# Kernel optimization log

Measured on AMD Instinct MI355X. Metric: run time of the kernel, lower is better.

The kernel has to match this reference:

```python
import jax, jax.numpy as jnp
import numpy as np

R = 16  # z_dim
_TRIU = np.triu_indices(R, 1)  # static index pair for plucker coords


def plucker_coords(u, v):
    # L2-normalised Plucker coordinates of span{u, v}; last dim r -> r*(r-1)//2
    outer = u[..., :, None] * v[..., None, :]
    anti = outer - jnp.swapaxes(outer, -1, -2)
    pc = anti[..., _TRIU[0], _TRIU[1]]
    nrm = jnp.linalg.norm(pc, axis=-1, keepdims=True)
    return pc / jnp.maximum(nrm, 1e-8)


def setup_inputs() -> dict:
    key = jax.random.key(0)
    ks = jax.random.split(key, 9)
    B, L, D, Z, P, H = 4, 256, 128, 16, 120, 256
    in_dim = 2 * D + 2 * Z + 3 * P + 2  # 650
    h = jax.random.normal(ks[0], (B, L, D), dtype=jnp.float32)
    z = jax.random.normal(ks[1], (B, L, Z), dtype=jnp.float32)
    p = jax.random.normal(ks[2], (B, L, P), dtype=jnp.float32)
    seq_mask = jax.random.randint(ks[3], (B, L), 0, 2).astype(bool)
    canon_mask = jax.random.randint(ks[4], (B, L, L), 0, 2).astype(bool)
    W1 = jax.random.normal(ks[5], (in_dim, H), dtype=jnp.float32) / np.sqrt(in_dim)
    b1 = jnp.zeros((H,), dtype=jnp.float32)
    W2 = jax.random.normal(ks[6], (H, 1), dtype=jnp.float32) / np.sqrt(H)
    b2 = jnp.zeros((1,), dtype=jnp.float32)
    return {"h": h, "z": z, "p": p, "seq_mask": seq_mask, "canon_mask": canon_mask,
            "W1": W1, "b1": b1, "W2": W2, "b2": b2}


def reference(h, z, p, seq_mask, canon_mask, W1, b1, W2, b2):
    B, L, _ = h.shape
    pos = jnp.arange(L, dtype=h.dtype)
    dist = jnp.abs(pos[:, None] - pos[None, :]) / max(L, 1)  # [L, L]
    dist = jnp.broadcast_to(dist[None, :, :, None], (B, L, L, 1))
    canon_f = canon_mask.astype(h.dtype)[..., None]  # [B, L, L, 1]

    h_i = jnp.broadcast_to(h[:, :, None, :], (B, L, L, h.shape[-1]))
    h_j = jnp.broadcast_to(h[:, None, :, :], (B, L, L, h.shape[-1]))
    z_i = jnp.broadcast_to(z[:, :, None, :], (B, L, L, z.shape[-1]))
    z_j = jnp.broadcast_to(z[:, None, :, :], (B, L, L, z.shape[-1]))
    p_i = jnp.broadcast_to(p[:, :, None, :], (B, L, L, p.shape[-1]))
    p_j = jnp.broadcast_to(p[:, None, :, :], (B, L, L, p.shape[-1]))
    p_ij = plucker_coords(z_i, z_j)  # [B, L, L, 120]

    feat = jnp.concatenate([h_i, h_j, z_i, z_j, p_i, p_j, p_ij, dist, canon_f], axis=-1)
    hdn = jax.nn.gelu(feat @ W1 + b1, approximate=False)
    e_pair = (hdn @ W2 + b2)[..., 0]  # [B, L, L]
    e_pair = (e_pair + jnp.swapaxes(e_pair, 1, 2)) * 0.5
    valid = seq_mask[:, :, None] & seq_mask[:, None, :]
    return jnp.where(valid, e_pair, jnp.asarray(30000.0, e_pair.dtype))
```

## Files before the change

### kernel.cpp

```cpp
#include <hip/hip_runtime.h>
#include <hip/hip_bf16.h>
#include <stdint.h>

#define BB     4
#define L_SEQ  256
#define DIM_H  128
#define DIM_Z  16
#define DIM_P  120
#define HID    256
#define TI     16
#define TJ     8
#define NPAIR  (TI*TJ)

typedef __attribute__((ext_vector_type(8))) short short8;
typedef __attribute__((ext_vector_type(4))) float f32x4;

__device__ __forceinline__ int imin(int a, int b){ return a < b ? a : b; }

struct Triu { int a[128]; int b[128]; };
static constexpr Triu make_triu(){
  Triu t{}; int k=0;
  for (int a=0;a<16;a++) for (int b=a+1;b<16;b++){ t.a[k]=a; t.b[k]=b; ++k; }
  for (;k<128;k++){ t.a[k]=0; t.b[k]=0; }
  return t;
}
static constexpr Triu TRIU = make_triu();

__device__ __forceinline__ short f2bf(float f){
  union { __hip_bfloat16 h; short s; } u;
  u.h = __float2bfloat16(f);
  return u.s;
}

__device__ __forceinline__ float bf2f(short s){
  union { float f; uint32_t u; } x;
  x.u = ((uint32_t)(uint16_t)s) << 16;
  return x.f;
}

__device__ __forceinline__ float gelu_fast(float x){
  float s = fmaf(0.42550f, x, 0.5f);
  s = fminf(fmaxf(s, 0.0f), 1.0f);
  return x * s;
}

template<int CTRL>
__device__ __forceinline__ float ror_add(float x){
  int xi = __float_as_int(x);
  int yi = __builtin_amdgcn_update_dpp(xi, xi, CTRL, 0xF, 0xF, false);
  return x + __int_as_float(yi);
}
__device__ __forceinline__ float reduce16(float x){
  x = ror_add<0x121>(x);
  x = ror_add<0x122>(x);
  x = ror_add<0x124>(x);
  x = ror_add<0x128>(x);
  return x;
}

__global__ __launch_bounds__(256) void k_prep(
    const uint32_t* __restrict__ seq_words, const float* __restrict__ W1,
    int* __restrict__ flag, int* __restrict__ vi, int* __restrict__ nv,
    short* __restrict__ W1pT)
{
  const int blk = blockIdx.x, tid = threadIdx.x;
  if (blk < BB){
    const int lane = tid & 63, w = tid >> 6;
    __shared__ int det[4];
    __shared__ int wc[4];
    uint32_t vdet = seq_words[tid] & 0xFFFFFF00u;
    unsigned long long bm = __ballot(vdet != 0u);
    if (lane == 0) det[w] = (bm != 0ull) ? 1 : 0;
    __syncthreads();
    const bool bytes = (det[0] | det[1] | det[2] | det[3]) != 0;
    if (blk == 0 && tid == 0) *flag = bytes ? 1 : 0;

    const int b = blk, i = tid;
    bool s;
    if (bytes) s = ((const unsigned char*)seq_words)[b*L_SEQ + i] != 0;
    else       s = ((const int*)          seq_words)[b*L_SEQ + i] != 0;
    unsigned long long m = __ballot(s);
    if (lane == 0) wc[w] = __popcll(m);
    __syncthreads();
    int base = 0;
    for (int x = 0; x < w; x++) base += wc[x];
    unsigned long long lower = (1ull << lane) - 1ull;
    int pos = base + __popcll(m & lower);
    if (s) vi[b*L_SEQ + pos] = i;
    if (i == 0) nv[b] = wc[0] + wc[1] + wc[2] + wc[3];
  } else {
    int idx = (blk - BB)*256 + tid;
    int k = idx & 127, n = idx >> 7;
    float v = 0.f;
    if (k < 120)      v = W1[(528+k)*HID + n];
    else if (k==120)  v = W1[648*HID + n];
    else if (k==121)  v = W1[649*HID + n];
    W1pT[n*128 + k] = f2bf(v);
  }
}

__global__ __launch_bounds__(256) void k1_precompute(
    const float* __restrict__ hbuf, const float* __restrict__ zbuf, const float* __restrict__ pbuf,
    const float* __restrict__ W1, const float* __restrict__ b1,
    const int* __restrict__ vi, const int* __restrict__ nv,
    float* __restrict__ Ai, float* __restrict__ Cj)
{
  const int bid = (blockIdx.x * 165) & 511;
  const int b = bid >> 7;
  const int p = bid & 127;
  const int nvb = nv[b];
  if (2*p >= nvb) return;
  const int r0 = vi[b*L_SEQ + 2*p];
  const int r1 = vi[b*L_SEQ + imin(2*p + 1, nvb - 1)];
  const size_t g0 = (size_t)(b*L_SEQ + r0), g1 = (size_t)(b*L_SEQ + r1);

  const int hcol = threadIdx.x;
  float a0, a1, c0, c1;
  a0 = a1 = b1[hcol];
  c0 = c1 = 0.f;

  const float* h0 = hbuf + g0*DIM_H;  const float* h1 = hbuf + g1*DIM_H;
  for (int k=0;k<DIM_H;k++){
    float wa = W1[k*HID + hcol], wc = W1[(128+k)*HID + hcol];
    a0 = fmaf(h0[k], wa, a0); c0 = fmaf(h0[k], wc, c0);
    a1 = fmaf(h1[k], wa, a1); c1 = fmaf(h1[k], wc, c1);
  }
  const float* z0 = zbuf + g0*DIM_Z;  const float* z1 = zbuf + g1*DIM_Z;
  for (int k=0;k<DIM_Z;k++){
    float wa = W1[(256+k)*HID + hcol], wc = W1[(272+k)*HID + hcol];
    a0 = fmaf(z0[k], wa, a0); c0 = fmaf(z0[k], wc, c0);
    a1 = fmaf(z1[k], wa, a1); c1 = fmaf(z1[k], wc, c1);
  }
  const float* p0 = pbuf + g0*DIM_P;  const float* p1 = pbuf + g1*DIM_P;
  for (int k=0;k<DIM_P;k++){
    float wa = W1[(288+k)*HID + hcol], wc = W1[(408+k)*HID + hcol];
    a0 = fmaf(p0[k], wa, a0); c0 = fmaf(p0[k], wc, c0);
    a1 = fmaf(p1[k], wa, a1); c1 = fmaf(p1[k], wc, c1);
  }
  Ai[g0*HID + hcol] = a0;  Cj[g0*HID + hcol] = c0;
  Ai[g1*HID + hcol] = a1;  Cj[g1*HID + hcol] = c1;
}

#define PCCOORD(T) f2bf((u[TRIU.a[(T)]]*v[TRIU.b[(T)]] - u[TRIU.b[(T)]]*v[TRIU.a[(T)]])*inv)
#define PC_CHUNK4(BASE) { \
  _Pragma("unroll") \
  for (int c_=0;c_<4;c_++){ \
    _Pragma("unroll") \
    for (int e_=0;e_<8;e_++){ pk[c_][e_] = PCCOORD((BASE) + c_*8 + e_); } } }

__global__ __launch_bounds__(512, 4) void k2_pair(
    const float* __restrict__ zbuf, const void* __restrict__ canon_raw,
    const float* __restrict__ Ai, const float* __restrict__ Cj,
    const short* __restrict__ W1pT, const float* __restrict__ W2,
    const int* __restrict__ flag_p, const int* __restrict__ vi, const int* __restrict__ nv,
    float* __restrict__ e_out)
{
  const int bid = (blockIdx.x * 997) & 2047;
  const int b  = bid >> 9;
  const int it = (bid >> 5) & 15;
  const int jt = bid & 31;
  const int i0 = it*TI, j0 = jt*TJ;
  const int nvb = nv[b];
  if (i0 >= nvb || j0 >= nvb) return;
  const int tid = threadIdx.x, lane = tid & 63, w = tid >> 6;
  const int brow = b*L_SEQ;

  short8 bfrag[2][4];
  {
    int g = lane >> 4, col = lane & 15;
    int n0 = (2*w+0)*16 + col, n1 = (2*w+1)*16 + col;
    #pragma unroll
    for (int ks=0; ks<4; ks++){
      bfrag[0][ks] = *reinterpret_cast<const short8*>(W1pT + n0*128 + ks*32 + g*8);
      bfrag[1][ks] = *reinterpret_cast<const short8*>(W1pT + n1*128 + ks*32 + g*8);
    }
  }

  __shared__ __align__(16) short pc_lds[NPAIR*128];
  __shared__ short ai_lds[TI*264];
  __shared__ short cj_lds[TJ*264];
  __shared__ float z_lds[(TI+TJ)*17];
  __shared__ float w2_lds[HID];
  __shared__ float epart[NPAIR*9];
  __shared__ int io_lds[TI];
  __shared__ int jo_lds[TJ];

  if (tid < TI)              io_lds[tid]    = vi[brow + imin(i0 + tid,      nvb-1)];
  else if (tid < TI+TJ)      jo_lds[tid-TI] = vi[brow + imin(j0 + (tid-TI), nvb-1)];
  __syncthreads();

  for (int idx = tid; idx < TI*HID; idx += 512){ int r = idx>>8, c = idx&255; ai_lds[r*264+c] = f2bf(Ai[(size_t)(brow+io_lds[r])*HID + c]); }
  for (int idx = tid; idx < TJ*HID; idx += 512){ int r = idx>>8, c = idx&255; cj_lds[r*264+c] = f2bf(Cj[(size_t)(brow+jo_lds[r])*HID + c]); }
  for (int idx = tid; idx < TI*DIM_Z; idx += 512){ int r = idx>>4, c = idx&15; z_lds[r*17+c] = zbuf[(size_t)(brow+io_lds[r])*DIM_Z + c]; }
  for (int idx = tid; idx < TJ*DIM_Z; idx += 512){ int r = idx>>4, c = idx&15; z_lds[(TI+r)*17+c] = zbuf[(size_t)(brow+jo_lds[r])*DIM_Z + c]; }
  if (tid < HID) w2_lds[tid] = W2[tid];
  __syncthreads();

  {
    const int p  = tid & 127;
    const int h  = tid >> 7;
    const int il = p >> 3, jl = p & 7;
    float u[16], v[16];
    #pragma unroll
    for (int a=0;a<16;a++) u[a] = z_lds[il*17+a];
    #pragma unroll
    for (int a=0;a<16;a++) v[a] = z_lds[(TI+jl)*17+a];
    float du=0.f, dv=0.f, uv=0.f;
    #pragma unroll
    for (int a=0;a<16;a++){ du=fmaf(u[a],u[a],du); dv=fmaf(v[a],v[a],dv); uv=fmaf(u[a],v[a],uv); }
    float q = fmaxf(du*dv - uv*uv, 1e-16f);
    float inv = __builtin_amdgcn_rsqf(q);

    short8 pk[4];
    if (h == 0)      PC_CHUNK4(0)
    else if (h == 1) PC_CHUNK4(32)
    else if (h == 2) PC_CHUNK4(64)
    else {
      #pragma unroll
      for (int c_=0;c_<3;c_++){
        #pragma unroll
        for (int e_=0;e_<8;e_++){ pk[c_][e_] = PCCOORD(96 + c_*8 + e_); }
      }
      int gi = io_lds[il], gj = jo_lds[jl];
      float dist = fabsf((float)(gi - gj)) * (1.0f/256.0f);
      float canon;
      if (*flag_p) canon = (((const unsigned char*)canon_raw)[(brow+gi)*L_SEQ + gj] != 0) ? 1.f : 0.f;
      else         canon = (((const int*)          canon_raw)[(brow+gi)*L_SEQ + gj] != 0) ? 1.f : 0.f;
      short8 last;
      last[0] = f2bf(dist); last[1] = f2bf(canon);
      #pragma unroll
      for (int e_=2;e_<8;e_++) last[e_] = (short)0;
      pk[3] = last;
    }
    char* pcb = (char*)pc_lds;
    const int rowbase = p*256 + h*64;
    #pragma unroll
    for (int c_=0;c_<4;c_++){
      int off = (rowbase + c_*16) ^ ((p&7)<<4);
      *reinterpret_cast<short8*>(pcb + off) = pk[c_];
    }
  }
  __syncthreads();

  {
    const int g = lane >> 4, col = lane & 15;
    const int n0 = (2*w+0)*16 + col, n1 = (2*w+1)*16 + col;
    const float w2v0 = w2_lds[n0], w2v1 = w2_lds[n1];
    const char* pcb = (const char*)pc_lds;

    for (int s=0; s<8; s++){
      short8 afrag[4];
      const int p = s*16 + col;
      #pragma unroll
      for (int ks=0; ks<4; ks++){
        int off = (p*256 + (ks*4+g)*16) ^ ((p&7)<<4);
        afrag[ks] = *reinterpret_cast<const short8*>(pcb + off);
      }
      f32x4 acc0 = {0.f,0.f,0.f,0.f}, acc1 = {0.f,0.f,0.f,0.f};
      #pragma unroll
      for (int ks=0; ks<4; ks++){
        acc0 = __builtin_amdgcn_mfma_f32_16x16x32_bf16(afrag[ks], bfrag[0][ks], acc0, 0,0,0);
        acc1 = __builtin_amdgcn_mfma_f32_16x16x32_bf16(afrag[ks], bfrag[1][ks], acc1, 0,0,0);
      }
      const int i_l = 2*s + (g>>1);
      const float ai0 = bf2f(ai_lds[i_l*264 + n0]);
      const float ai1 = bf2f(ai_lds[i_l*264 + n1]);
      float psum[4];
      #pragma unroll
      for (int r=0;r<4;r++){
        int m  = g*4 + r;
        int jl = m & 7;
        float cj0 = bf2f(cj_lds[jl*264 + n0]);
        float cj1 = bf2f(cj_lds[jl*264 + n1]);
        float pre0 = acc0[r] + ai0 + cj0;
        float pre1 = acc1[r] + ai1 + cj1;
        psum[r] = fmaf(gelu_fast(pre0), w2v0, gelu_fast(pre1)*w2v1);
      }
      #pragma unroll
      for (int r=0;r<4;r++) psum[r] = reduce16(psum[r]);
      if (col == 0){
        #pragma unroll
        for (int r=0;r<4;r++) epart[(s*16 + g*4 + r)*9 + w] = psum[r];
      }
    }
  }
  __syncthreads();

  if (tid < NPAIR){
    float sum = 0.f;
    #pragma unroll
    for (int ww=0; ww<8; ww++) sum += epart[tid*9 + ww];
    e_out[(size_t)(brow + io_lds[tid>>3])*L_SEQ + jo_lds[tid&7]] = sum;
  }
}

__global__ __launch_bounds__(256) void k3_sym(
    const float* __restrict__ e_in, const void* __restrict__ seq_raw,
    const float* __restrict__ b2, const int* __restrict__ flag_p,
    float* __restrict__ out)
{
  int idx = blockIdx.x*256 + threadIdx.x;
  int b = idx >> 14, rem = idx & 16383, i = rem >> 6, j4 = (rem & 63) << 2;
  bool si, sj[4];
  if (*flag_p){
    const unsigned char* s8 = (const unsigned char*)seq_raw;
    si = s8[b*L_SEQ+i] != 0;
    #pragma unroll
    for (int t=0;t<4;t++) sj[t] = s8[b*L_SEQ+j4+t] != 0;
  } else {
    const int* s32 = (const int*)seq_raw;
    si = s32[b*L_SEQ+i] != 0;
    #pragma unroll
    for (int t=0;t<4;t++) sj[t] = s32[b*L_SEQ+j4+t] != 0;
  }
  const float bias = b2[0];
  f32x4 o;
  #pragma unroll
  for (int t=0;t<4;t++){
    float val = 30000.0f;
    if (si && sj[t]){
      float e1 = e_in[((size_t)b*L_SEQ+i)*L_SEQ + j4+t];
      float e2 = e_in[((size_t)b*L_SEQ+j4+t)*L_SEQ + i];
      val = 0.5f*(e1 + e2) + bias;
    }
    o[t] = val;
  }
  *reinterpret_cast<f32x4*>(out + ((size_t)b*L_SEQ+i)*L_SEQ + j4) = o;
}

extern "C" void kernel_launch(void* const* d_in, const int* in_sizes, int n_in,
                              void* d_out, int out_size, void* d_ws, size_t ws_size,
                              hipStream_t stream)
{
  const float* hbuf  = (const float*)d_in[0];
  const float* zbuf  = (const float*)d_in[1];
  const float* pbuf  = (const float*)d_in[2];
  const void*  seq   = d_in[3];
  const void*  canon = d_in[4];
  const float* W1    = (const float*)d_in[5];
  const float* b1    = (const float*)d_in[6];
  const float* W2    = (const float*)d_in[7];
  const float* b2    = (const float*)d_in[8];

  char* ws = (char*)d_ws;
  float* Ai   = (float*)(ws);
  float* Cj   = (float*)(ws + (1<<20));
  short* W1pT = (short*)(ws + (2<<20));
  float* e_ws = (float*)(ws + (2<<20) + 65536);
  int*   flag = (int*)  (ws + (2<<20) + 65536 + (1<<20));
  int*   vi   = (int*)  (ws + (2<<20) + 65536 + (1<<20) + 256);
  int*   nv   = (int*)  (ws + (2<<20) + 65536 + (1<<20) + 256 + 4096);

  k_prep<<<BB + 128, 256, 0, stream>>>((const uint32_t*)seq, W1, flag, vi, nv, W1pT);
  k1_precompute<<<BB*128, 256, 0, stream>>>(hbuf, zbuf, pbuf, W1, b1, vi, nv, Ai, Cj);
  k2_pair<<<BB*16*32, 512, 0, stream>>>(zbuf, canon, Ai, Cj, W1pT, W2, flag, vi, nv, e_ws);
  k3_sym<<<(BB*L_SEQ*L_SEQ/4)/256, 256, 0, stream>>>(e_ws, seq, b2, flag, (float*)d_out);
}
```

Baseline: 57.20 us.

## Merge prep kernels and fuse symmetrization into pair kernel via atomics

Folds the prep, per-row precompute, and output initialization into one kernel launch, splitting the K dimension of the row projections across two thread halves with an LDS reduction. The separate symmetrization kernel is removed: the pair kernel atomically adds half of each pair energy into both (i,j) and (j,i) of the output, which is pre-filled with the bias or the 30000 mask value. This drops two launches and the intermediate energy buffer round trip, at the cost of float atomics and nondeterministic summation order.

```diff
diff --git a/kernel.cpp b/kernel.cpp
--- a/kernel.cpp
+++ b/kernel.cpp
@@ -58,87 +58,121 @@
   return x;
 }
 
-__global__ __launch_bounds__(256) void k_prep(
+__global__ __launch_bounds__(512) void k_prepA(
     const uint32_t* __restrict__ seq_words, const float* __restrict__ W1,
+    const float* __restrict__ b1, const float* __restrict__ b2,
+    const float* __restrict__ hbuf, const float* __restrict__ zbuf, const float* __restrict__ pbuf,
     int* __restrict__ flag, int* __restrict__ vi, int* __restrict__ nv,
-    short* __restrict__ W1pT)
+    short* __restrict__ W1pT, float* __restrict__ Ai, float* __restrict__ Cj,
+    float* __restrict__ out)
 {
   const int blk = blockIdx.x, tid = threadIdx.x;
-  if (blk < BB){
-    const int lane = tid & 63, w = tid >> 6;
-    __shared__ int det[4];
-    __shared__ int wc[4];
-    uint32_t vdet = seq_words[tid] & 0xFFFFFF00u;
-    unsigned long long bm = __ballot(vdet != 0u);
-    if (lane == 0) det[w] = (bm != 0ull) ? 1 : 0;
-    __syncthreads();
-    const bool bytes = (det[0] | det[1] | det[2] | det[3]) != 0;
-    if (blk == 0 && tid == 0) *flag = bytes ? 1 : 0;
-
-    const int b = blk, i = tid;
-    bool s;
-    if (bytes) s = ((const unsigned char*)seq_words)[b*L_SEQ + i] != 0;
-    else       s = ((const int*)          seq_words)[b*L_SEQ + i] != 0;
-    unsigned long long m = __ballot(s);
-    if (lane == 0) wc[w] = __popcll(m);
-    __syncthreads();
-    int base = 0;
-    for (int x = 0; x < w; x++) base += wc[x];
-    unsigned long long lower = (1ull << lane) - 1ull;
-    int pos = base + __popcll(m & lower);
-    if (s) vi[b*L_SEQ + pos] = i;
-    if (i == 0) nv[b] = wc[0] + wc[1] + wc[2] + wc[3];
-  } else {
-    int idx = (blk - BB)*256 + tid;
+  const int lane = tid & 63, w = tid >> 6;
+
+  if (blk >= 4 && blk < 68){
+    int idx = (blk - 4)*512 + tid;
     int k = idx & 127, n = idx >> 7;
     float v = 0.f;
     if (k < 120)      v = W1[(528+k)*HID + n];
     else if (k==120)  v = W1[648*HID + n];
     else if (k==121)  v = W1[649*HID + n];
     W1pT[n*128 + k] = f2bf(v);
-  }
-}
-
-__global__ __launch_bounds__(256) void k1_precompute(
-    const float* __restrict__ hbuf, const float* __restrict__ zbuf, const float* __restrict__ pbuf,
-    const float* __restrict__ W1, const float* __restrict__ b1,
-    const int* __restrict__ vi, const int* __restrict__ nv,
-    float* __restrict__ Ai, float* __restrict__ Cj)
-{
-  const int bid = (blockIdx.x * 165) & 511;
-  const int b = bid >> 7;
-  const int p = bid & 127;
-  const int nvb = nv[b];
-  if (2*p >= nvb) return;
-  const int r0 = vi[b*L_SEQ + 2*p];
-  const int r1 = vi[b*L_SEQ + imin(2*p + 1, nvb - 1)];
-  const size_t g0 = (size_t)(b*L_SEQ + r0), g1 = (size_t)(b*L_SEQ + r1);
-
-  const int hcol = threadIdx.x;
-  float a0, a1, c0, c1;
-  a0 = a1 = b1[hcol];
-  c0 = c1 = 0.f;
-
-  const float* h0 = hbuf + g0*DIM_H;  const float* h1 = hbuf + g1*DIM_H;
-  for (int k=0;k<DIM_H;k++){
-    float wa = W1[k*HID + hcol], wc = W1[(128+k)*HID + hcol];
-    a0 = fmaf(h0[k], wa, a0); c0 = fmaf(h0[k], wc, c0);
-    a1 = fmaf(h1[k], wa, a1); c1 = fmaf(h1[k], wc, c1);
-  }
-  const float* z0 = zbuf + g0*DIM_Z;  const float* z1 = zbuf + g1*DIM_Z;
-  for (int k=0;k<DIM_Z;k++){
-    float wa = W1[(256+k)*HID + hcol], wc = W1[(272+k)*HID + hcol];
-    a0 = fmaf(z0[k], wa, a0); c0 = fmaf(z0[k], wc, c0);
-    a1 = fmaf(z1[k], wa, a1); c1 = fmaf(z1[k], wc, c1);
-  }
-  const float* p0 = pbuf + g0*DIM_P;  const float* p1 = pbuf + g1*DIM_P;
-  for (int k=0;k<DIM_P;k++){
-    float wa = W1[(288+k)*HID + hcol], wc = W1[(408+k)*HID + hcol];
-    a0 = fmaf(p0[k], wa, a0); c0 = fmaf(p0[k], wc, c0);
-    a1 = fmaf(p1[k], wa, a1); c1 = fmaf(p1[k], wc, c1);
-  }
-  Ai[g0*HID + hcol] = a0;  Cj[g0*HID + hcol] = c0;
-  Ai[g1*HID + hcol] = a1;  Cj[g1*HID + hcol] = c1;
+    return;
+  }
+
+  __shared__ int detf;
+  __shared__ int wc[4];
+  __shared__ float par[2][2][2][HID];
+  if (tid == 0) detf = 0;
+  __syncthreads();
+  if (tid < 256 && (seq_words[tid] & 0xFFFFFF00u)) atomicOr(&detf, 1);
+  __syncthreads();
+  const bool bytes = detf != 0;
+  const unsigned char* s8  = (const unsigned char*)seq_words;
+  const int*           s32 = (const int*)seq_words;
+
+  if (blk < 4){
+    if (blk == 0 && tid == 0) *flag = bytes ? 1 : 0;
+    const int b = blk, i = tid;
+    bool s = false;
+    if (tid < 256) s = bytes ? (s8[b*L_SEQ + i] != 0) : (s32[b*L_SEQ + i] != 0);
+    unsigned long long m = __ballot(s);
+    if (tid < 256 && lane == 0) wc[w] = __popcll(m);
+    __syncthreads();
+    if (tid < 256){
+      int base = 0;
+      for (int x = 0; x < w; x++) base += wc[x];
+      unsigned long long lower = (1ull << lane) - 1ull;
+      int pos = base + __popcll(m & lower);
+      if (s) vi[b*L_SEQ + pos] = i;
+      if (i == 0) nv[b] = wc[0] + wc[1] + wc[2] + wc[3];
+    }
+    return;
+  }
+
+  if (blk < 196){
+    const float bias2 = b2[0];
+    int idx = (blk - 68)*512 + tid;
+    int b = idx >> 14, i = (idx >> 6) & 255, j4 = (idx & 63) << 2;
+    bool si = bytes ? (s8[b*L_SEQ+i] != 0) : (s32[b*L_SEQ+i] != 0);
+    f32x4 o;
+    #pragma unroll
+    for (int t=0;t<4;t++){
+      bool sj = bytes ? (s8[b*L_SEQ+j4+t] != 0) : (s32[b*L_SEQ+j4+t] != 0);
+      o[t] = (si && sj) ? bias2 : 30000.0f;
+    }
+    *reinterpret_cast<f32x4*>(out + ((size_t)b*L_SEQ+i)*L_SEQ + j4) = o;
+    return;
+  }
+
+  {
+    const int p2 = blk - 196;
+    const int row0 = 2*p2, row1 = row0 + 1;
+    bool v0 = bytes ? (s8[row0] != 0) : (s32[row0] != 0);
+    bool v1 = bytes ? (s8[row1] != 0) : (s32[row1] != 0);
+    if (!v0 && !v1) return;
+
+    const int ks = tid >> 8;
+    const int hcol = tid & 255;
+    float a0, a1, c0, c1;
+    if (ks == 0){
+      float bias = b1[hcol];
+      a0 = a1 = bias; c0 = c1 = 0.f;
+      const float* h0 = hbuf + (size_t)row0*DIM_H;
+      const float* h1 = h0 + DIM_H;
+      for (int k=0;k<DIM_H;k++){
+        float wa = W1[k*HID + hcol], wcv = W1[(128+k)*HID + hcol];
+        a0 = fmaf(h0[k], wa, a0); c0 = fmaf(h0[k], wcv, c0);
+        a1 = fmaf(h1[k], wa, a1); c1 = fmaf(h1[k], wcv, c1);
+      }
+    } else {
+      a0 = a1 = c0 = c1 = 0.f;
+      const float* z0 = zbuf + (size_t)row0*DIM_Z;
+      const float* z1 = z0 + DIM_Z;
+      for (int k=0;k<DIM_Z;k++){
+        float wa = W1[(256+k)*HID + hcol], wcv = W1[(272+k)*HID + hcol];
+        a0 = fmaf(z0[k], wa, a0); c0 = fmaf(z0[k], wcv, c0);
+        a1 = fmaf(z1[k], wa, a1); c1 = fmaf(z1[k], wcv, c1);
+      }
+      const float* p0 = pbuf + (size_t)row0*DIM_P;
+      const float* p1 = p0 + DIM_P;
+      for (int k=0;k<DIM_P;k++){
+        float wa = W1[(288+k)*HID + hcol], wcv = W1[(408+k)*HID + hcol];
+        a0 = fmaf(p0[k], wa, a0); c0 = fmaf(p0[k], wcv, c0);
+        a1 = fmaf(p1[k], wa, a1); c1 = fmaf(p1[k], wcv, c1);
+      }
+    }
+    par[ks][0][0][hcol] = a0;  par[ks][0][1][hcol] = c0;
+    par[ks][1][0][hcol] = a1;  par[ks][1][1][hcol] = c1;
+    __syncthreads();
+    if (tid < 256){
+      const int h = tid;
+      Ai[(size_t)row0*HID + h] = par[0][0][0][h] + par[1][0][0][h];
+      Cj[(size_t)row0*HID + h] = par[0][0][1][h] + par[1][0][1][h];
+      Ai[(size_t)row1*HID + h] = par[0][1][0][h] + par[1][1][0][h];
+      Cj[(size_t)row1*HID + h] = par[0][1][1][h] + par[1][1][1][h];
+    }
+  }
 }
 
 #define PCCOORD(T) f2bf((u[TRIU.a[(T)]]*v[TRIU.b[(T)]] - u[TRIU.b[(T)]]*v[TRIU.a[(T)]])*inv)
@@ -153,7 +187,7 @@
     const float* __restrict__ Ai, const float* __restrict__ Cj,
     const short* __restrict__ W1pT, const float* __restrict__ W2,
     const int* __restrict__ flag_p, const int* __restrict__ vi, const int* __restrict__ nv,
-    float* __restrict__ e_out)
+    float* __restrict__ out)
 {
   const int bid = (blockIdx.x * 997) & 2047;
   const int b  = bid >> 9;
@@ -290,42 +324,14 @@
     float sum = 0.f;
     #pragma unroll
     for (int ww=0; ww<8; ww++) sum += epart[tid*9 + ww];
-    e_out[(size_t)(brow + io_lds[tid>>3])*L_SEQ + jo_lds[tid&7]] = sum;
-  }
-}
-
-__global__ __launch_bounds__(256) void k3_sym(
-    const float* __restrict__ e_in, const void* __restrict__ seq_raw,
-    const float* __restrict__ b2, const int* __restrict__ flag_p,
-    float* __restrict__ out)
-{
-  int idx = blockIdx.x*256 + threadIdx.x;
-  int b = idx >> 14, rem = idx & 16383, i = rem >> 6, j4 = (rem & 63) << 2;
-  bool si, sj[4];
-  if (*flag_p){
-    const unsigned char* s8 = (const unsigned char*)seq_raw;
-    si = s8[b*L_SEQ+i] != 0;
-    #pragma unroll
-    for (int t=0;t<4;t++) sj[t] = s8[b*L_SEQ+j4+t] != 0;
-  } else {
-    const int* s32 = (const int*)seq_raw;
-    si = s32[b*L_SEQ+i] != 0;
-    #pragma unroll
-    for (int t=0;t<4;t++) sj[t] = s32[b*L_SEQ+j4+t] != 0;
-  }
-  const float bias = b2[0];
-  f32x4 o;
-  #pragma unroll
-  for (int t=0;t<4;t++){
-    float val = 30000.0f;
-    if (si && sj[t]){
-      float e1 = e_in[((size_t)b*L_SEQ+i)*L_SEQ + j4+t];
-      float e2 = e_in[((size_t)b*L_SEQ+j4+t)*L_SEQ + i];
-      val = 0.5f*(e1 + e2) + bias;
-    }
-    o[t] = val;
-  }
-  *reinterpret_cast<f32x4*>(out + ((size_t)b*L_SEQ+i)*L_SEQ + j4) = o;
+    const int ci = i0 + (tid>>3), cj = j0 + (tid&7);
+    if (ci < nvb && cj < nvb){
+      const int gi = io_lds[tid>>3], gj = jo_lds[tid&7];
+      const float hsum = 0.5f * sum;
+      atomicAdd(&out[(size_t)(brow + gi)*L_SEQ + gj], hsum);
+      atomicAdd(&out[(size_t)(brow + gj)*L_SEQ + gi], hsum);
+    }
+  }
 }
 
 extern "C" void kernel_launch(void* const* d_in, const int* in_sizes, int n_in,
@@ -346,13 +352,13 @@
   float* Ai   = (float*)(ws);
   float* Cj   = (float*)(ws + (1<<20));
   short* W1pT = (short*)(ws + (2<<20));
-  float* e_ws = (float*)(ws + (2<<20) + 65536);
-  int*   flag = (int*)  (ws + (2<<20) + 65536 + (1<<20));
-  int*   vi   = (int*)  (ws + (2<<20) + 65536 + (1<<20) + 256);
-  int*   nv   = (int*)  (ws + (2<<20) + 65536 + (1<<20) + 256 + 4096);
-
-  k_prep<<<BB + 128, 256, 0, stream>>>((const uint32_t*)seq, W1, flag, vi, nv, W1pT);
-  k1_precompute<<<BB*128, 256, 0, stream>>>(hbuf, zbuf, pbuf, W1, b1, vi, nv, Ai, Cj);
-  k2_pair<<<BB*16*32, 512, 0, stream>>>(zbuf, canon, Ai, Cj, W1pT, W2, flag, vi, nv, e_ws);
-  k3_sym<<<(BB*L_SEQ*L_SEQ/4)/256, 256, 0, stream>>>(e_ws, seq, b2, flag, (float*)d_out);
-}
+  int*   flag = (int*)  (ws + (2<<20) + 65536);
+  int*   vi   = (int*)  (ws + (2<<20) + 65536 + 256);
+  int*   nv   = (int*)  (ws + (2<<20) + 65536 + 256 + 4096);
+
+  k_prepA<<<708, 512, 0, stream>>>((const uint32_t*)seq, W1, b1, b2,
+                                   hbuf, zbuf, pbuf,
+                                   flag, vi, nv, W1pT, Ai, Cj, (float*)d_out);
+  k2_pair<<<BB*16*32, 512, 0, stream>>>(zbuf, canon, Ai, Cj, W1pT, W2,
+                                        flag, vi, nv, (float*)d_out);
+}
```

After: 49.55 us, median of 2. 13.4% less time.
